# Performance work log

Hardware: AMD Instinct MI355X
Metric: run time of the kernel (lower is better)

The kernel has to match this reference:

```python
import jax, jax.numpy as jnp
import numpy as np

B, N, E, H = 8, 1024, 768, 12
HD = E // H  # head_dim = 64
EPS = 1e-5


def setup_inputs() -> dict:
    key = jax.random.key(0)
    ks = jax.random.split(key, 3)
    x = jax.random.normal(ks[0], (B, N, E), dtype=jnp.float32)
    # Packed in-projection like torch nn.MultiheadAttention (in_proj_weight [3E, E])
    w_qkv = jax.random.normal(ks[1], (3 * E, E), dtype=jnp.float32) * (1.0 / np.sqrt(E))
    b_qkv = jnp.zeros((3 * E,), dtype=jnp.float32)
    w_out = jax.random.normal(ks[2], (E, E), dtype=jnp.float32) * (1.0 / np.sqrt(E))
    b_out = jnp.zeros((E,), dtype=jnp.float32)
    ln_g = jnp.ones((E,), dtype=jnp.float32)
    ln_b = jnp.zeros((E,), dtype=jnp.float32)
    return {"x": x, "ln_g": ln_g, "ln_b": ln_b, "w_qkv": w_qkv,
            "b_qkv": b_qkv, "w_out": w_out, "b_out": b_out}


def reference(x, ln_g, ln_b, w_qkv, b_qkv, w_out, b_out):
    # LayerNorm over last dim (eps=1e-5, elementwise affine)
    mu = jnp.mean(x, axis=-1, keepdims=True)
    var = jnp.mean(jnp.square(x - mu), axis=-1, keepdims=True)
    xn = (x - mu) * jax.lax.rsqrt(var + EPS) * ln_g + ln_b

    # Packed QKV projection: torch does x @ in_proj_weight.T + in_proj_bias
    qkv = jnp.einsum('bne,fe->bnf', xn, w_qkv) + b_qkv  # [B, N, 3E]
    q, k, v = jnp.split(qkv, 3, axis=-1)
    # Split heads -> [B, H, N, HD]
    q = q.reshape(B, N, H, HD).transpose(0, 2, 1, 3)
    k = k.reshape(B, N, H, HD).transpose(0, 2, 1, 3)
    v = v.reshape(B, N, H, HD).transpose(0, 2, 1, 3)

    scale = 1.0 / np.sqrt(HD)
    scores = jnp.einsum('bhqd,bhkd->bhqk', q * scale, k)  # [B, H, N, N]
    attn = jax.nn.softmax(scores, axis=-1)
    # (attn_dropout=0.0; need_weights=True forces this manual path in torch,
    #  averaged weights attn.mean(axis=1) are computed but not returned here
    #  since return_attention_map defaults to False)
    ctx = jnp.einsum('bhqk,bhkd->bhqd', attn, v)  # [B, H, N, HD]
    ctx = ctx.transpose(0, 2, 1, 3).reshape(B, N, E)

    out = jnp.einsum('bne,fe->bnf', ctx, w_out) + b_out  # out_proj
    return out
```

## Files before the change

### kernel.cpp

```cpp
#include <hip/hip_runtime.h>
#include <hip/hip_bf16.h>
#include <stdint.h>

#define B_ 8
#define N_ 1024
#define E_ 768
#define H_ 12
#define HD_ 64
#define M_ (B_ * N_)

typedef __attribute__((ext_vector_type(8))) short bf8_t;
typedef __attribute__((ext_vector_type(4))) float f4_t;

__device__ __forceinline__ unsigned short f2bf(float f) {
  unsigned u = __builtin_bit_cast(unsigned, f);
  unsigned r = (u + 0x7fffu + ((u >> 16) & 1u)) >> 16;
  return (unsigned short)r;
}

__device__ __forceinline__ unsigned cvt_pk_bf16(float lo, float hi) {
  unsigned r;
  asm("v_cvt_pk_bf16_f32 %0, %1, %2" : "=v"(r) : "v"(lo), "v"(hi));
  return r;
}

__device__ __forceinline__ float exp2_hw(float x) {
  float r;
  asm("v_exp_f32 %0, %1" : "=v"(r) : "v"(x));
  return r;
}

__device__ __forceinline__ void load_lds16(const void* g, void* l) {
  __builtin_amdgcn_global_load_lds(
      (__attribute__((address_space(1))) void*)(g),
      (__attribute__((address_space(3))) void*)(l), 16, 0, 0);
}

__device__ __forceinline__ int swz(int row) {
  return ((row ^ (row >> 3)) & 7) << 3;
}

#define F3(a, b, c) fmaxf(fmaxf((a), (b)), (c))

__global__ void k_cast_bf16(const float* __restrict__ in,
                            unsigned short* __restrict__ out, int n4) {
  int i = blockIdx.x * blockDim.x + threadIdx.x;
  if (i < n4) {
    float4 v = ((const float4*)in)[i];
    ushort4 o;
    o.x = f2bf(v.x); o.y = f2bf(v.y); o.z = f2bf(v.z); o.w = f2bf(v.w);
    ((ushort4*)out)[i] = o;
  }
}

__global__ __launch_bounds__(192) void k_ln(const float* __restrict__ x,
                                            const float* __restrict__ g,
                                            const float* __restrict__ bta,
                                            unsigned short* __restrict__ xn) {
  int row = blockIdx.x;
  int t = threadIdx.x;
  float4 v = ((const float4*)(x + (size_t)row * E_))[t];
  float s = v.x + v.y + v.z + v.w;
  float s2 = v.x * v.x + v.y * v.y + v.z * v.z + v.w * v.w;
  for (int off = 32; off; off >>= 1) {
    s += __shfl_xor(s, off, 64);
    s2 += __shfl_xor(s2, off, 64);
  }
  __shared__ float red[6];
  int lane = t & 63, wv = t >> 6;
  if (lane == 0) { red[wv] = s; red[3 + wv] = s2; }
  __syncthreads();
  s = red[0] + red[1] + red[2];
  s2 = red[3] + red[4] + red[5];
  float mu = s * (1.0f / E_);
  float var = s2 * (1.0f / E_) - mu * mu;
  float rstd = rsqrtf(var + 1e-5f);
  float4 gg = ((const float4*)g)[t];
  float4 bb = ((const float4*)bta)[t];
  ushort4 o;
  o.x = f2bf((v.x - mu) * rstd * gg.x + bb.x);
  o.y = f2bf((v.y - mu) * rstd * gg.y + bb.y);
  o.z = f2bf((v.z - mu) * rstd * gg.z + bb.z);
  o.w = f2bf((v.w - mu) * rstd * gg.w + bb.w);
  ((ushort4*)(xn + (size_t)row * E_))[t] = o;
}

template <int EPI>
__global__ __launch_bounds__(256) void k_gemm_bt(
    const unsigned short* __restrict__ A,
    const unsigned short* __restrict__ W,
    const float* __restrict__ bias,
    unsigned short* __restrict__ oQ, unsigned short* __restrict__ oK,
    unsigned short* __restrict__ oVt, float* __restrict__ oF,
    int K, int Nf) {
  __shared__ unsigned short Al[2][128 * 64];
  __shared__ unsigned short Bl[2][128 * 64];
  const int nbx = Nf >> 7;
  const int nwg = nbx << 6;
  const int orig = blockIdx.y * nbx + blockIdx.x;
  const int id = (orig & 7) * (nwg >> 3) + (orig >> 3);
  const int n0 = (id % nbx) * 128, m0 = (id / nbx) * 128;
  const int tid = threadIdx.x;
  const int lane = tid & 63, wv = tid >> 6;
  const int wr = wv >> 1, wc = wv & 1;
  const int g = lane >> 4, l15 = lane & 15;
  f4_t acc[4][4] = {};

  auto stage = [&](int k0, int buf) {
#pragma unroll
    for (int i = 0; i < 4; ++i) {
      int e = (i * 256 + tid) * 8;
      int r = e >> 6;
      int c = (e & 63) ^ swz(r);
      load_lds16(A + (size_t)(m0 + r) * K + (k0 + c), &Al[buf][e]);
      load_lds16(W + (size_t)(n0 + r) * K + (k0 + c), &Bl[buf][e]);
    }
  };

  stage(0, 0);
  __syncthreads();
  int cur = 0;

  for (int k0 = 0; k0 < K; k0 += 64) {
    if (k0 + 64 < K) stage(k0 + 64, cur ^ 1);
    const unsigned short* Ac = Al[cur];
    const unsigned short* Bc = Bl[cur];
#pragma unroll
    for (int kk = 0; kk < 2; ++kk) {
      bf8_t af[4], bfr[4];
#pragma unroll
      for (int mi = 0; mi < 4; ++mi) {
        int ar = wr * 64 + mi * 16 + l15;
        af[mi] = *(const bf8_t*)&Ac[(ar * 64 + kk * 32 + g * 8) ^ swz(ar)];
      }
#pragma unroll
      for (int ni = 0; ni < 4; ++ni) {
        int br = wc * 64 + ni * 16 + l15;
        bfr[ni] = *(const bf8_t*)&Bc[(br * 64 + kk * 32 + g * 8) ^ swz(br)];
      }
#pragma unroll
      for (int mi = 0; mi < 4; ++mi)
#pragma unroll
        for (int ni = 0; ni < 4; ++ni)
          acc[mi][ni] = __builtin_amdgcn_mfma_f32_16x16x32_bf16(
              af[mi], bfr[ni], acc[mi][ni], 0, 0, 0);
    }
    __syncthreads();
    cur ^= 1;
  }

#pragma unroll
  for (int mi = 0; mi < 4; ++mi) {
#pragma unroll
    for (int ni = 0; ni < 4; ++ni) {
      int f = n0 + wc * 64 + ni * 16 + l15;
      float bs = bias[f];
#pragma unroll
      for (int i = 0; i < 4; ++i) {
        int m = m0 + wr * 64 + mi * 16 + g * 4 + i;
        float val = acc[mi][ni][i] + bs;
        if (EPI == 0) {
          int bb = m >> 10, n = m & 1023;
          int which = f / E_;
          int e2 = f - which * E_;
          int h = e2 >> 6, d = e2 & 63;
          size_t qk = (((size_t)bb * H_ + h) * N_ + n) * HD_ + d;
          if (which == 0) oQ[qk] = f2bf(val * 0.1803368801f);
          else if (which == 1) oK[qk] = f2bf(val);
          else oVt[(((size_t)bb * H_ + h) * HD_ + d) * N_ + n] = f2bf(val);
        } else {
          oF[(size_t)m * E_ + f] = val;
        }
      }
    }
  }
}

__global__ __launch_bounds__(256) void k_attn(
    const unsigned short* __restrict__ Q,
    const unsigned short* __restrict__ Kb,
    const unsigned short* __restrict__ Vt,
    unsigned short* __restrict__ ctx) {
  __shared__ unsigned short Kl[2][64 * 64];
  __shared__ unsigned short Vl[2][64 * 64];
  __shared__ unsigned short Pl[4][16 * 64];
  const int bh = blockIdx.x;
  const int qt = blockIdx.y;
  const int tid = threadIdx.x;
  const int lane = tid & 63, wv = tid >> 6;
  const int g = lane >> 4, l15 = lane & 15;

  const unsigned short* Qp = Q + ((size_t)bh * N_ + qt * 64 + wv * 16) * HD_;
  bf8_t qf[2];
#pragma unroll
  for (int kk = 0; kk < 2; ++kk)
    qf[kk] = *(const bf8_t*)&Qp[(size_t)l15 * HD_ + kk * 32 + g * 8];

  f4_t o[4] = {};
  float mrow = -1e30f, lrow = 0.f;
  const unsigned short* Kbase = Kb + (size_t)bh * N_ * HD_;
  const unsigned short* Vbase = Vt + (size_t)bh * HD_ * N_;

  auto stage = [&](int t, int buf) {
#pragma unroll
    for (int i = 0; i < 2; ++i) {
      int e = (i * 256 + tid) * 8;
      int r = e >> 6;
      int c = (e & 63) ^ swz(r);
      load_lds16(Kbase + (size_t)(t * 64 + r) * HD_ + c, &Kl[buf][e]);
      load_lds16(Vbase + (size_t)r * N_ + (t * 64 + c), &Vl[buf][e]);
    }
  };

  stage(0, 0);
  __syncthreads();
  int cur = 0;
  unsigned short* Pw = &Pl[wv][0];

  for (int t = 0; t < 16; ++t) {
    if (t + 1 < 16) stage(t + 1, cur ^ 1);
    const unsigned short* Klc = Kl[cur];
    const unsigned short* Vlc = Vl[cur];

    f4_t s[4] = {};
    __builtin_amdgcn_s_setprio(1);
#pragma unroll
    for (int ni = 0; ni < 4; ++ni) {
      int krow = ni * 16 + l15;
#pragma unroll
      for (int kk = 0; kk < 2; ++kk) {
        bf8_t kf = *(const bf8_t*)&Klc[(krow * 64 + kk * 32 + g * 8) ^ swz(krow)];
        s[ni] = __builtin_amdgcn_mfma_f32_16x16x32_bf16(kf, qf[kk], s[ni], 0, 0, 0);
      }
    }
    __builtin_amdgcn_s_setprio(0);

    float t0 = F3(s[0][0], s[0][1], s[0][2]);
    float t1 = F3(s[0][3], s[1][0], s[1][1]);
    float t2 = F3(s[1][2], s[1][3], s[2][0]);
    float t3 = F3(s[2][1], s[2][2], s[2][3]);
    float t4 = F3(s[3][0], s[3][1], s[3][2]);
    float mx = fmaxf(F3(F3(t0, t1, t2), t3, t4), s[3][3]);

    if (!__all(mx - mrow <= 8.0f)) {
      float Mx = fmaxf(mx, __shfl_xor(mx, 16, 64));
      Mx = fmaxf(Mx, __shfl_xor(Mx, 32, 64));
      float mnew = fmaxf(mrow, Mx);
      float al = exp2_hw(mrow - mnew);
      lrow *= al;
#pragma unroll
      for (int di = 0; di < 4; ++di)
#pragma unroll
        for (int i = 0; i < 4; ++i) o[di][i] *= al;
      mrow = mnew;
    }

    float p0  = exp2_hw(s[0][0] - mrow), p1  = exp2_hw(s[0][1] - mrow);
    float p2  = exp2_hw(s[0][2] - mrow), p3  = exp2_hw(s[0][3] - mrow);
    float p4  = exp2_hw(s[1][0] - mrow), p5  = exp2_hw(s[1][1] - mrow);
    float p6  = exp2_hw(s[1][2] - mrow), p7  = exp2_hw(s[1][3] - mrow);
    float p8  = exp2_hw(s[2][0] - mrow), p9  = exp2_hw(s[2][1] - mrow);
    float p10 = exp2_hw(s[2][2] - mrow), p11 = exp2_hw(s[2][3] - mrow);
    float p12 = exp2_hw(s[3][0] - mrow), p13 = exp2_hw(s[3][1] - mrow);
    float p14 = exp2_hw(s[3][2] - mrow), p15 = exp2_hw(s[3][3] - mrow);
    float a0 = p0 + p1, a1 = p2 + p3, a2 = p4 + p5, a3 = p6 + p7;
    float a4 = p8 + p9, a5 = p10 + p11, a6 = p12 + p13, a7 = p14 + p15;
    float b0 = a0 + a1, b1 = a2 + a3, b2 = a4 + a5, b3 = a6 + a7;
    lrow += (b0 + b1) + (b2 + b3);

    {
      uint2 pk;
      pk.x = cvt_pk_bf16(p0, p1);   pk.y = cvt_pk_bf16(p2, p3);
      *(uint2*)&Pw[l15 * 64 + ((0 * 16 + g * 4) ^ ((l15 & 7) << 3))] = pk;
      pk.x = cvt_pk_bf16(p4, p5);   pk.y = cvt_pk_bf16(p6, p7);
      *(uint2*)&Pw[l15 * 64 + ((1 * 16 + g * 4) ^ ((l15 & 7) << 3))] = pk;
      pk.x = cvt_pk_bf16(p8, p9);   pk.y = cvt_pk_bf16(p10, p11);
      *(uint2*)&Pw[l15 * 64 + ((2 * 16 + g * 4) ^ ((l15 & 7) << 3))] = pk;
      pk.x = cvt_pk_bf16(p12, p13); pk.y = cvt_pk_bf16(p14, p15);
      *(uint2*)&Pw[l15 * 64 + ((3 * 16 + g * 4) ^ ((l15 & 7) << 3))] = pk;
    }
    asm volatile("s_waitcnt lgkmcnt(0)" ::: "memory");
    __builtin_amdgcn_sched_barrier(0);

    __builtin_amdgcn_s_setprio(1);
#pragma unroll
    for (int kk = 0; kk < 2; ++kk) {
      bf8_t pf = *(const bf8_t*)&Pw[l15 * 64 + ((kk * 32 + g * 8) ^ ((l15 & 7) << 3))];
#pragma unroll
      for (int di = 0; di < 4; ++di) {
        int vrow = di * 16 + l15;
        bf8_t vf = *(const bf8_t*)&Vlc[(vrow * 64 + kk * 32 + g * 8) ^ swz(vrow)];
        o[di] = __builtin_amdgcn_mfma_f32_16x16x32_bf16(vf, pf, o[di], 0, 0, 0);
      }
    }
    __builtin_amdgcn_s_setprio(0);

    __syncthreads();
    cur ^= 1;
  }

  lrow += __shfl_xor(lrow, 16, 64);
  lrow += __shfl_xor(lrow, 32, 64);
  float rinv = 1.0f / lrow;
#pragma unroll
  for (int di = 0; di < 4; ++di) {
    uint2 pk;
    pk.x = cvt_pk_bf16(o[di][0] * rinv, o[di][1] * rinv);
    pk.y = cvt_pk_bf16(o[di][2] * rinv, o[di][3] * rinv);
    int oe = l15 * 64 + ((di * 16 + g * 4) ^ ((l15 & 7) << 3));
    *(uint2*)&Pw[oe] = pk;
  }
  asm volatile("s_waitcnt lgkmcnt(0)" ::: "memory");
  __builtin_amdgcn_sched_barrier(0);

  const int bb = bh / H_, h = bh - bb * H_;
  const int rr = lane >> 2, cb = (lane & 3) * 16;
#pragma unroll
  for (int m2 = 0; m2 < 2; ++m2) {
    int e = rr * 64 + ((cb + 8 * m2) ^ ((rr & 7) << 3));
    bf8_t val = *(const bf8_t*)&Pw[e];
    unsigned short* dst =
        ctx + ((size_t)bb * N_ + qt * 64 + wv * 16 + rr) * E_ + h * HD_ + cb + 8 * m2;
    *(bf8_t*)dst = val;
  }
}

extern "C" void kernel_launch(void* const* d_in, const int* in_sizes, int n_in,
                              void* d_out, int out_size, void* d_ws, size_t ws_size,
                              hipStream_t stream) {
  const float* x     = (const float*)d_in[0];
  const float* ln_g  = (const float*)d_in[1];
  const float* ln_b  = (const float*)d_in[2];
  const float* w_qkv = (const float*)d_in[3];
  const float* b_qkv = (const float*)d_in[4];
  const float* w_out = (const float*)d_in[5];
  const float* b_out = (const float*)d_in[6];
  float* out = (float*)d_out;

  char* ws = (char*)d_ws;
  const size_t SZ = (size_t)M_ * E_ * 2;
  unsigned short* xn    = (unsigned short*)(ws);
  unsigned short* qb    = (unsigned short*)(ws + SZ);
  unsigned short* kbuf  = (unsigned short*)(ws + 2 * SZ);
  unsigned short* vtb   = (unsigned short*)(ws + 3 * SZ);
  unsigned short* ctx   = (unsigned short*)(ws + 4 * SZ);
  unsigned short* wqkvb = (unsigned short*)(ws + 5 * SZ);
  unsigned short* woutb = (unsigned short*)(ws + 5 * SZ + (size_t)3 * E_ * E_ * 2);

  int n1 = 3 * E_ * E_ / 4;
  k_cast_bf16<<<(n1 + 255) / 256, 256, 0, stream>>>(w_qkv, wqkvb, n1);
  int n2 = E_ * E_ / 4;
  k_cast_bf16<<<(n2 + 255) / 256, 256, 0, stream>>>(w_out, woutb, n2);

  k_ln<<<M_, 192, 0, stream>>>(x, ln_g, ln_b, xn);

  k_gemm_bt<0><<<dim3(18, 64), 256, 0, stream>>>(xn, wqkvb, b_qkv, qb, kbuf, vtb,
                                                 nullptr, E_, 3 * E_);
  k_attn<<<dim3(96, 16), 256, 0, stream>>>(qb, kbuf, vtb, ctx);
  k_gemm_bt<1><<<dim3(6, 64), 256, 0, stream>>>(ctx, woutb, b_out, nullptr, nullptr,
                                                nullptr, out, E_, E_);
}
```

Before: 155.5 us.

## Keep two tiles in flight with vmcnt-based waits in GEMM and attention

Both the GEMM and attention loops now issue loads for two tiles ahead and use explicit s_waitcnt vmcnt(N) plus a raw s_barrier, instead of __syncthreads, which waits for every outstanding load. This lets the next tile's global-to-LDS transfers stay in flight while the current tile is computed, hiding more memory latency. It relies on correct vmcnt counts matching the number of loads per stage (8 for the GEMM, 4 for attention). A miscount would produce a race.

```diff
diff --git a/kernel.cpp b/kernel.cpp
--- a/kernel.cpp
+++ b/kernel.cpp
@@ -35,6 +35,17 @@
       (__attribute__((address_space(1))) void*)(g),
       (__attribute__((address_space(3))) void*)(l), 16, 0, 0);
 }
+
+#define WAITV(N)                                        \
+  asm volatile("s_waitcnt vmcnt(" #N ")" ::: "memory"); \
+  __builtin_amdgcn_sched_barrier(0);                    \
+  __builtin_amdgcn_s_barrier();                         \
+  __builtin_amdgcn_sched_barrier(0);
+
+#define BAR2()                          \
+  __builtin_amdgcn_sched_barrier(0);    \
+  __builtin_amdgcn_s_barrier();         \
+  __builtin_amdgcn_sched_barrier(0);
 
 __device__ __forceinline__ int swz(int row) {
   return ((row ^ (row >> 3)) & 7) << 3;
@@ -117,12 +128,13 @@
     }
   };
 
+  const int NT = K >> 6;
   stage(0, 0);
-  __syncthreads();
-  int cur = 0;
-
-  for (int k0 = 0; k0 < K; k0 += 64) {
-    if (k0 + 64 < K) stage(k0 + 64, cur ^ 1);
+  stage(64, 1);
+
+  for (int t = 0; t < NT; ++t) {
+    const int cur = t & 1;
+    if (t + 1 < NT) { WAITV(8); } else { WAITV(0); }
     const unsigned short* Ac = Al[cur];
     const unsigned short* Bc = Bl[cur];
 #pragma unroll
@@ -145,8 +157,8 @@
           acc[mi][ni] = __builtin_amdgcn_mfma_f32_16x16x32_bf16(
               af[mi], bfr[ni], acc[mi][ni], 0, 0, 0);
     }
-    __syncthreads();
-    cur ^= 1;
+    BAR2();
+    if (t + 2 < NT) stage((t + 2) << 6, cur);
   }
 
 #pragma unroll
@@ -213,12 +225,12 @@
   };
 
   stage(0, 0);
-  __syncthreads();
-  int cur = 0;
+  stage(1, 1);
   unsigned short* Pw = &Pl[wv][0];
 
   for (int t = 0; t < 16; ++t) {
-    if (t + 1 < 16) stage(t + 1, cur ^ 1);
+    const int cur = t & 1;
+    if (t + 1 < 16) { WAITV(4); } else { WAITV(0); }
     const unsigned short* Klc = Kl[cur];
     const unsigned short* Vlc = Vl[cur];
 
@@ -295,8 +307,8 @@
     }
     __builtin_amdgcn_s_setprio(0);
 
-    __syncthreads();
-    cur ^= 1;
+    BAR2();
+    if (t + 2 < 16) stage(t + 2, cur);
   }
 
   lrow += __shfl_xor(lrow, 16, 64);
```

Result: no change. 154.9 us (-0.4%).
